# Kernel tuning notes

Measured on AMD Instinct MI355X. Metric: run time of the kernel, lower is better.

Reference implementation:

```python
import jax, jax.numpy as jnp
import numpy as np

H = 2048   # hidden_dim
E = 8      # num_experts
K = 2      # top_k
N = 4096   # tokens


def setup_inputs() -> dict:
    key = jax.random.key(0)
    ks = jax.random.split(key, 8)
    scale = 0.02
    return {
        "x": jax.random.normal(ks[0], (N, H), dtype=jnp.float32),
        # gate: torch Linear(H, E) -> weight [E, H], bias [E]
        "gate_W": jax.random.normal(ks[1], (E, H), dtype=jnp.float32) * scale,
        "gate_b": jnp.zeros((E,), dtype=jnp.float32),
        # per-expert 2-layer MLP; stored as [E, in, out] for direct einsum
        "W1": jax.random.normal(ks[2], (E, H, H), dtype=jnp.float32) * scale,
        "b1": jnp.zeros((E, H), dtype=jnp.float32),
        "W2": jax.random.normal(ks[3], (E, H, H), dtype=jnp.float32) * scale,
        "b2": jnp.zeros((E, H), dtype=jnp.float32),
    }


def reference(x, gate_W, gate_b, W1, b1, W2, b2):
    # gate softmax over experts: [N, E]
    gate_scores = jax.nn.softmax(x @ gate_W.T + gate_b, axis=-1)
    topk_scores, topk_idx = jax.lax.top_k(gate_scores, K)  # [N, K]
    n = x.shape[0]
    # combine weights: score at selected experts, 0 elsewhere -> [N, E]
    combine = jnp.zeros_like(gate_scores).at[
        jnp.arange(n)[:, None], topk_idx
    ].set(topk_scores)
    # dense per-expert MLP: h [N, E, H]
    h = jax.nn.relu(jnp.einsum('nh,ehf->nef', x, W1) + b1)
    out_e = jnp.einsum('nef,efg->neg', h, W2) + b2  # [N, E, H]
    aggregated = jnp.einsum('ne,neh->nh', combine, out_e)  # [N, H]
    return aggregated, gate_scores
```

## Files before the change

kernel.cpp:

```cpp
#include <hip/hip_runtime.h>
#include <hip/hip_bf16.h>

#define N_TOK 4096
#define HD    2048
#define NE    8

#define BM 128
#define BN 256
#define BK 32
#define NKS (HD/BK)
#define MAXROWS (N_TOK*2 + NE*BM)
#define TMAX (MAXROWS/BM)
#define NNT  (HD/BN)
#define NWG  (TMAX*NNT)
#define TSZ  ((BM+BN)*BK*2)

#define NCOPY 64

typedef __attribute__((ext_vector_type(4))) float f32x4;
typedef __attribute__((ext_vector_type(8))) short short8;
typedef __attribute__((ext_vector_type(8))) unsigned short ushort8;

typedef unsigned short u16;
typedef unsigned int   u32;


__device__ __forceinline__ float bf2f(u16 u) {
  union { u32 i; float f; } c; c.i = ((u32)u) << 16; return c.f;
}
__device__ __forceinline__ u16 f2bf(float f) {
  u32 x = __float_as_uint(f);
  u32 r = (x + 0x7fffu + ((x >> 16) & 1u)) >> 16;
  return (u16)r;
}

__device__ __forceinline__ void gload_lds16(const void* gsrc, void* ldst) {
  __builtin_amdgcn_global_load_lds(
      (const __attribute__((address_space(1))) u32*)gsrc,
      (__attribute__((address_space(3))) u32*)ldst, 16, 0, 0);
}

__global__ __launch_bounds__(256) void convert_transpose_kernel(
    const float* __restrict__ W1, const float* __restrict__ W2,
    u16* __restrict__ W1T, u16* __restrict__ W2T) {
  __shared__ float tile[64][65];
  int z = blockIdx.z;
  const float* W = (z < NE) ? W1 : W2;
  u16* WT = (z < NE) ? W1T : W2T;
  int e = z & 7;
  size_t ebase = (size_t)e * HD * HD;
  int n0 = blockIdx.x * 64;
  int k0 = blockIdx.y * 64;
  int t = threadIdx.x;
  int l = t & 63, w = t >> 6;
  #pragma unroll
  for (int jr = 0; jr < 4; ++jr) {
    int r = w*16 + jr*4 + (l >> 4);
    int cc = (l & 15) * 4;
    f32x4 v = *reinterpret_cast<const f32x4*>(W + ebase + (size_t)(k0 + r) * HD + n0 + cc);
    tile[r][cc+0] = v[0]; tile[r][cc+1] = v[1];
    tile[r][cc+2] = v[2]; tile[r][cc+3] = v[3];
  }
  __syncthreads();
  #pragma unroll
  for (int ps = 0; ps < 2; ++ps) {
    int np = ps*32 + (t >> 3);
    int kc = (t & 7) * 8;
    ushort8 v;
    #pragma unroll
    for (int j = 0; j < 8; ++j) v[j] = f2bf(tile[kc + j][np]);
    *reinterpret_cast<ushort8*>(WT + ebase + (size_t)(n0 + np) * HD + k0 + kc) = v;
  }
}

__global__ __launch_bounds__(256) void gate_kernel(
    const float* __restrict__ x, const float* __restrict__ gW, const float* __restrict__ gb,
    float* __restrict__ gate_out, int* __restrict__ cnt,
    int* __restrict__ picks, float* __restrict__ wts) {
  int wid = (blockIdx.x << 2) + (threadIdx.x >> 6);
  int lane = threadIdx.x & 63;
  int copy = blockIdx.x & (NCOPY-1);
  const float* xr = x + (size_t)wid * HD;
  float s[NE] = {};
  for (int k = 0; k < HD; k += 256) {
    f32x4 xv = *reinterpret_cast<const f32x4*>(xr + k + lane*4);
    #pragma unroll
    for (int e = 0; e < NE; ++e) {
      f32x4 wv = *reinterpret_cast<const f32x4*>(gW + (size_t)e*HD + k + lane*4);
      s[e] += xv[0]*wv[0] + xv[1]*wv[1] + xv[2]*wv[2] + xv[3]*wv[3];
    }
  }
  #pragma unroll
  for (int e = 0; e < NE; ++e) {
    float v = s[e];
    #pragma unroll
    for (int off = 32; off > 0; off >>= 1) v += __shfl_xor(v, off);
    s[e] = v + gb[e];
  }
  float mx = s[0];
  #pragma unroll
  for (int e = 1; e < NE; ++e) mx = fmaxf(mx, s[e]);
  float sum = 0.f;
  #pragma unroll
  for (int e = 0; e < NE; ++e) { s[e] = expf(s[e] - mx); sum += s[e]; }
  float inv = 1.f / sum;
  #pragma unroll
  for (int e = 0; e < NE; ++e) s[e] *= inv;
  int e0 = 0; float v0 = s[0];
  #pragma unroll
  for (int e = 1; e < NE; ++e) if (s[e] > v0) { v0 = s[e]; e0 = e; }
  int e1 = -1; float v1 = -1.f;
  #pragma unroll
  for (int e = 0; e < NE; ++e) if (e != e0 && s[e] > v1) { v1 = s[e]; e1 = e; }
  if (lane == 0) {
    #pragma unroll
    for (int e = 0; e < NE; ++e) gate_out[(size_t)wid*NE + e] = s[e];
    int p0 = atomicAdd(&cnt[copy*8 + e0], 1);
    int p1 = atomicAdd(&cnt[copy*8 + e1], 1);
    picks[wid*2]   = (p0 << 9) | (copy << 3) | e0;
    picks[wid*2+1] = (p1 << 9) | (copy << 3) | e1;
    wts[wid*2]   = v0;
    wts[wid*2+1] = v1;
  }
}

__global__ void scan_kernel(int* meta) {
  int e = threadIdx.x;
  if (e < NE) {
    int run = 0;
    for (int c = 0; c < NCOPY; ++c) {
      meta[512 + c*8 + e] = run;
      run += meta[c*8 + e];
    }
    meta[1024 + e] = run;
  }
}

__global__ void fill_kernel(const int* __restrict__ picks, const int* __restrict__ meta,
                            int* __restrict__ slot, int* __restrict__ rowTok) {
  int i = blockIdx.x * 256 + threadIdx.x;
  if (i >= N_TOK*2) return;
  int p = picks[i];
  int e = p & 7, c = (p >> 3) & (NCOPY-1), pos = p >> 9;
  int base = 0;
  #pragma unroll
  for (int ee = 0; ee < NE; ++ee)
    if (ee < e) base += ((meta[1024+ee] + BM - 1) >> 7) << 7;
  int row = base + meta[512 + c*8 + e] + pos;
  slot[i] = row;
  rowTok[row] = i >> 1;
}

__global__ __launch_bounds__(256) void gather_kernel(
    const float* __restrict__ x, const int* __restrict__ rowTok,
    u16* __restrict__ Xg) {
  int row = blockIdx.x;
  int tok = rowTok[row];
  int c = threadIdx.x * 8;
  ushort8 v;
  if (tok >= 0) {
    const f32x4* src = reinterpret_cast<const f32x4*>(x + (size_t)tok * HD + c);
    f32x4 a = src[0], b = src[1];
    #pragma unroll
    for (int j = 0; j < 4; ++j) { v[j] = f2bf(a[j]); v[4+j] = f2bf(b[j]); }
  } else {
    #pragma unroll
    for (int j = 0; j < 8; ++j) v[j] = 0;
  }
  *reinterpret_cast<ushort8*>(Xg + (size_t)row * HD + c) = v;
}

__device__ __forceinline__ void stage_tile(char* ldsbuf, const u16* Ak, const u16* Bk, int tid) {
  {
    int r = tid >> 2;
    int c = (tid & 3) ^ ((r >> 1) & 3);
    gload_lds16(Ak + (size_t)r*HD + c*8, ldsbuf + tid*16);
  }
  #pragma unroll
  for (int i = 0; i < 2; ++i) {
    int L = i*512 + tid;
    int r = L >> 2;
    int c = (L & 3) ^ ((r >> 1) & 3);
    gload_lds16(Bk + (size_t)r*HD + c*8, ldsbuf + BM*BK*2 + L*16);
  }
}

__device__ __forceinline__ void compute_ktile(
    const char* ldsA, const char* ldsB, f32x4 (&acc)[4][4],
    int wr, int wc, int l15, int lhi) {
  short8 af[4], bfr[4];
  #pragma unroll
  for (int m = 0; m < 4; ++m) {
    int r = wr*64 + m*16 + l15;
    int c = lhi ^ ((r >> 1) & 3);
    af[m] = *reinterpret_cast<const short8*>(ldsA + r*64 + c*16);
  }
  #pragma unroll
  for (int n = 0; n < 4; ++n) {
    int r = wc*64 + n*16 + l15;
    int c = lhi ^ ((r >> 1) & 3);
    bfr[n] = *reinterpret_cast<const short8*>(ldsB + r*64 + c*16);
  }
  #pragma unroll
  for (int m = 0; m < 4; ++m)
    #pragma unroll
    for (int n = 0; n < 4; ++n)
      acc[m][n] = __builtin_amdgcn_mfma_f32_16x16x32_bf16(af[m], bfr[n], acc[m][n], 0, 0, 0);
}

template<bool RELU>
__global__ __launch_bounds__(512, 4) void moe_gemm_kernel(
    const u16* __restrict__ A,
    const u16* __restrict__ WT,
    const float* __restrict__ bias,
    u16* __restrict__ Out,
    const int* __restrict__ tot) {
  int bid = blockIdx.x;
  int wg = (bid & 7) * (NWG/8) + (bid >> 3);
  int t  = wg >> 3;
  int nt = wg & 7;
  int tiles = 0, rows = 0, e = 0, tstart = 0, rbase = 0;
  #pragma unroll
  for (int i = 0; i < NE; ++i) {
    int tl = (tot[i] + BM - 1) >> 7;
    if (t >= tiles && t < tiles + tl) { e = i; tstart = tiles; rbase = rows; }
    tiles += tl; rows += tl << 7;
  }
  if (t >= tiles) return;
  int rowBase = rbase + (t - tstart) * BM;

  const u16* Ap = A + (size_t)rowBase * HD;
  const u16* Bp = WT + ((size_t)e * HD + (size_t)nt * BN) * HD;

  __shared__ char lds[3*TSZ];

  int tid = threadIdx.x;
  int lane = tid & 63;
  int wv = tid >> 6;
  int wr = wv >> 2, wc = wv & 3;
  int l15 = lane & 15, lhi = lane >> 4;

  f32x4 acc[4][4] = {};

  stage_tile(lds,       Ap,      Bp,      tid);
  stage_tile(lds + TSZ, Ap + BK, Bp + BK, tid);

  int rd = 0;
  for (int ks = 0; ks < NKS - 2; ++ks) {
    asm volatile("s_waitcnt vmcnt(3)" ::: "memory");
    __builtin_amdgcn_s_barrier();
    int wi = rd + 2; if (wi >= 3) wi -= 3;
    stage_tile(lds + wi*TSZ, Ap + (ks+2)*BK, Bp + (ks+2)*BK, tid);
    __builtin_amdgcn_sched_barrier(0);
    compute_ktile(lds + rd*TSZ, lds + rd*TSZ + BM*BK*2, acc, wr, wc, l15, lhi);
    if (++rd == 3) rd = 0;
  }
  asm volatile("s_waitcnt vmcnt(3)" ::: "memory");
  __builtin_amdgcn_s_barrier();
  compute_ktile(lds + rd*TSZ, lds + rd*TSZ + BM*BK*2, acc, wr, wc, l15, lhi);
  if (++rd == 3) rd = 0;
  asm volatile("s_waitcnt vmcnt(0)" ::: "memory");
  __builtin_amdgcn_s_barrier();
  compute_ktile(lds + rd*TSZ, lds + rd*TSZ + BM*BK*2, acc, wr, wc, l15, lhi);

  int orow = rowBase + wr*64;
  int ocol = nt*BN + wc*64;
  const float* bp = bias + (size_t)e * HD + ocol;
  #pragma unroll
  for (int n = 0; n < 4; ++n) {
    float bv = bp[n*16 + l15];
    #pragma unroll
    for (int m = 0; m < 4; ++m) {
      #pragma unroll
      for (int j = 0; j < 4; ++j) {
        float v = acc[m][n][j] + bv;
        if (RELU) v = fmaxf(v, 0.f);
        Out[(size_t)(orow + m*16 + lhi*4 + j) * HD + (ocol + n*16 + l15)] = f2bf(v);
      }
    }
  }
}

__global__ __launch_bounds__(256) void combine_kernel(
    const u16* __restrict__ Y, const int* __restrict__ slot,
    const float* __restrict__ wts, float* __restrict__ out) {
  int n = blockIdx.x;
  int r0 = slot[n*2], r1 = slot[n*2+1];
  float w0 = wts[n*2], w1 = wts[n*2+1];
  int c = threadIdx.x * 8;
  ushort8 y0 = *reinterpret_cast<const ushort8*>(Y + (size_t)r0*HD + c);
  ushort8 y1 = *reinterpret_cast<const ushort8*>(Y + (size_t)r1*HD + c);
  f32x4 o0, o1;
  #pragma unroll
  for (int j = 0; j < 4; ++j) {
    o0[j] = w0*bf2f(y0[j])   + w1*bf2f(y1[j]);
    o1[j] = w0*bf2f(y0[4+j]) + w1*bf2f(y1[4+j]);
  }
  f32x4* dst = reinterpret_cast<f32x4*>(out + (size_t)n*HD + c);
  dst[0] = o0; dst[1] = o1;
}

extern "C" void kernel_launch(void* const* d_in, const int* in_sizes, int n_in,
                              void* d_out, int out_size, void* d_ws, size_t ws_size,
                              hipStream_t stream) {
  const float* x     = (const float*)d_in[0];
  const float* gateW = (const float*)d_in[1];
  const float* gateb = (const float*)d_in[2];
  const float* W1    = (const float*)d_in[3];
  const float* b1    = (const float*)d_in[4];
  const float* W2    = (const float*)d_in[5];
  const float* b2    = (const float*)d_in[6];
  float* out      = (float*)d_out;
  float* gate_out = out + (size_t)N_TOK * HD;

  char* ws = (char*)d_ws;
  size_t o = 0;
  u16* W1T = (u16*)(ws + o); o += (size_t)NE*HD*HD*2;
  u16* W2T = (u16*)(ws + o); o += (size_t)NE*HD*HD*2;
  u16* Xg  = (u16*)(ws + o);
  u16* Y   = Xg;
  o += (size_t)MAXROWS*HD*2;
  u16* Hbuf = (u16*)(ws + o); o += (size_t)MAXROWS*HD*2;
  int*   meta   = (int*)(ws + o);   o += 8192;
  int*   picks  = (int*)(ws + o);   o += (size_t)N_TOK*2*4;
  float* wts    = (float*)(ws + o); o += (size_t)N_TOK*2*4;
  int*   slot   = (int*)(ws + o);   o += (size_t)N_TOK*2*4;
  int*   rowTok = (int*)(ws + o);   o += (size_t)MAXROWS*4;

  hipMemsetAsync(meta, 0, NCOPY*8*4, stream);
  hipMemsetAsync(rowTok, 0xFF, (size_t)MAXROWS*4, stream);

  convert_transpose_kernel<<<dim3(HD/64, HD/64, 2*NE), 256, 0, stream>>>(W1, W2, W1T, W2T);
  gate_kernel<<<N_TOK/4, 256, 0, stream>>>(x, gateW, gateb, gate_out, meta, picks, wts);
  scan_kernel<<<1, 64, 0, stream>>>(meta);
  fill_kernel<<<(N_TOK*2)/256, 256, 0, stream>>>(picks, meta, slot, rowTok);
  gather_kernel<<<MAXROWS, 256, 0, stream>>>(x, rowTok, Xg);
  moe_gemm_kernel<true ><<<dim3(NWG), 512, 0, stream>>>(Xg,   W1T, b1, Hbuf, meta + 1024);
  moe_gemm_kernel<false><<<dim3(NWG), 512, 0, stream>>>(Hbuf, W2T, b2, Y,    meta + 1024);
  combine_kernel<<<N_TOK, 256, 0, stream>>>(Y, slot, wts, out);
}
```

Baseline: 323.2 us.

## Deepen GEMM LDS pipeline to five buffers with split-phase interleaved loads and MFMAs

Moves the expert GEMM main loop from a 3-buffer, 2-ahead prefetch to a 5-buffer ring that prefetches 3 k-tiles ahead. Each k-step is split into two phases: LDS fragment reads and global-to-LDS loads are interleaved with half of the MFMAs, separated by extra barriers, and the MFMA sections run under raised s_setprio. The aim is to hide global load latency better and keep the matrix units busy. In exchange, occupancy is lowered (launch bounds 4 to 2 and more LDS per block), and the extra barriers per k-step add synchronisation cost.

```diff
diff --git a/kernel.cpp b/kernel.cpp
--- a/kernel.cpp
+++ b/kernel.cpp
@@ -14,6 +14,7 @@
 #define NNT  (HD/BN)
 #define NWG  (TMAX*NNT)
 #define TSZ  ((BM+BN)*BK*2)
+#define NBUF 5
 
 #define NCOPY 64
 
@@ -170,46 +171,20 @@
   *reinterpret_cast<ushort8*>(Xg + (size_t)row * HD + c) = v;
 }
 
-__device__ __forceinline__ void stage_tile(char* ldsbuf, const u16* Ak, const u16* Bk, int tid) {
-  {
-    int r = tid >> 2;
-    int c = (tid & 3) ^ ((r >> 1) & 3);
-    gload_lds16(Ak + (size_t)r*HD + c*8, ldsbuf + tid*16);
-  }
-  #pragma unroll
-  for (int i = 0; i < 2; ++i) {
-    int L = i*512 + tid;
-    int r = L >> 2;
-    int c = (L & 3) ^ ((r >> 1) & 3);
-    gload_lds16(Bk + (size_t)r*HD + c*8, ldsbuf + BM*BK*2 + L*16);
-  }
-}
-
-__device__ __forceinline__ void compute_ktile(
-    const char* ldsA, const char* ldsB, f32x4 (&acc)[4][4],
-    int wr, int wc, int l15, int lhi) {
-  short8 af[4], bfr[4];
-  #pragma unroll
-  for (int m = 0; m < 4; ++m) {
-    int r = wr*64 + m*16 + l15;
-    int c = lhi ^ ((r >> 1) & 3);
-    af[m] = *reinterpret_cast<const short8*>(ldsA + r*64 + c*16);
-  }
-  #pragma unroll
-  for (int n = 0; n < 4; ++n) {
-    int r = wc*64 + n*16 + l15;
-    int c = lhi ^ ((r >> 1) & 3);
-    bfr[n] = *reinterpret_cast<const short8*>(ldsB + r*64 + c*16);
-  }
-  #pragma unroll
-  for (int m = 0; m < 4; ++m)
-    #pragma unroll
-    for (int n = 0; n < 4; ++n)
-      acc[m][n] = __builtin_amdgcn_mfma_f32_16x16x32_bf16(af[m], bfr[n], acc[m][n], 0, 0, 0);
+__device__ __forceinline__ void stage_A(char* ldsbuf, const u16* Ak, int tid) {
+  int r = tid >> 2;
+  int c = (tid & 3) ^ ((r >> 1) & 3);
+  gload_lds16(Ak + (size_t)r*HD + c*8, ldsbuf + tid*16);
+}
+__device__ __forceinline__ void stage_B(char* ldsbuf, const u16* Bk, int tid, int i) {
+  int L = i*512 + tid;
+  int r = L >> 2;
+  int c = (L & 3) ^ ((r >> 1) & 3);
+  gload_lds16(Bk + (size_t)r*HD + c*8, ldsbuf + BM*BK*2 + L*16);
 }
 
 template<bool RELU>
-__global__ __launch_bounds__(512, 4) void moe_gemm_kernel(
+__global__ __launch_bounds__(512, 2) void moe_gemm_kernel(
     const u16* __restrict__ A,
     const u16* __restrict__ WT,
     const float* __restrict__ bias,
@@ -232,7 +207,7 @@
   const u16* Ap = A + (size_t)rowBase * HD;
   const u16* Bp = WT + ((size_t)e * HD + (size_t)nt * BN) * HD;
 
-  __shared__ char lds[3*TSZ];
+  __shared__ char lds[NBUF*TSZ];
 
   int tid = threadIdx.x;
   int lane = tid & 63;
@@ -242,26 +217,78 @@
 
   f32x4 acc[4][4] = {};
 
-  stage_tile(lds,       Ap,      Bp,      tid);
-  stage_tile(lds + TSZ, Ap + BK, Bp + BK, tid);
-
-  int rd = 0;
-  for (int ks = 0; ks < NKS - 2; ++ks) {
-    asm volatile("s_waitcnt vmcnt(3)" ::: "memory");
+  #pragma unroll
+  for (int p = 0; p < 3; ++p) {
+    stage_A(lds + p*TSZ, Ap + p*BK, tid);
+    stage_B(lds + p*TSZ, Bp + p*BK, tid, 0);
+    stage_B(lds + p*TSZ, Bp + p*BK, tid, 1);
+  }
+
+  int rd = 0, wi = 3;
+  for (int ks = 0; ks < NKS; ++ks) {
+    if (ks < NKS-2)       asm volatile("s_waitcnt vmcnt(6)" ::: "memory");
+    else if (ks == NKS-2) asm volatile("s_waitcnt vmcnt(3)" ::: "memory");
+    else                  asm volatile("s_waitcnt vmcnt(0)" ::: "memory");
     __builtin_amdgcn_s_barrier();
-    int wi = rd + 2; if (wi >= 3) wi -= 3;
-    stage_tile(lds + wi*TSZ, Ap + (ks+2)*BK, Bp + (ks+2)*BK, tid);
-    __builtin_amdgcn_sched_barrier(0);
-    compute_ktile(lds + rd*TSZ, lds + rd*TSZ + BM*BK*2, acc, wr, wc, l15, lhi);
-    if (++rd == 3) rd = 0;
-  }
-  asm volatile("s_waitcnt vmcnt(3)" ::: "memory");
-  __builtin_amdgcn_s_barrier();
-  compute_ktile(lds + rd*TSZ, lds + rd*TSZ + BM*BK*2, acc, wr, wc, l15, lhi);
-  if (++rd == 3) rd = 0;
-  asm volatile("s_waitcnt vmcnt(0)" ::: "memory");
-  __builtin_amdgcn_s_barrier();
-  compute_ktile(lds + rd*TSZ, lds + rd*TSZ + BM*BK*2, acc, wr, wc, l15, lhi);
+    __builtin_amdgcn_sched_barrier(0);
+
+    const char* bufA = lds + rd*TSZ;
+    const char* bufB = bufA + BM*BK*2;
+    char* wbuf = lds + wi*TSZ;
+    bool issue = (ks + 3 < NKS);
+    const u16* Aq = Ap + (ks+3)*BK;
+    const u16* Bq = Bp + (ks+3)*BK;
+
+    short8 af[4], bfr[4];
+    #pragma unroll
+    for (int m = 0; m < 4; ++m) {
+      int r = wr*64 + m*16 + l15;
+      int c = lhi ^ ((r >> 1) & 3);
+      af[m] = *reinterpret_cast<const short8*>(bufA + r*64 + c*16);
+    }
+    #pragma unroll
+    for (int n = 0; n < 2; ++n) {
+      int r = wc*64 + n*16 + l15;
+      int c = lhi ^ ((r >> 1) & 3);
+      bfr[n] = *reinterpret_cast<const short8*>(bufB + r*64 + c*16);
+    }
+    if (issue) { stage_A(wbuf, Aq, tid); stage_B(wbuf, Bq, tid, 0); }
+    __builtin_amdgcn_sched_barrier(0);
+    __builtin_amdgcn_s_barrier();
+    __builtin_amdgcn_sched_barrier(0);
+    __builtin_amdgcn_s_setprio(1);
+    #pragma unroll
+    for (int m = 0; m < 4; ++m)
+      #pragma unroll
+      for (int n = 0; n < 2; ++n)
+        acc[m][n] = __builtin_amdgcn_mfma_f32_16x16x32_bf16(af[m], bfr[n], acc[m][n], 0, 0, 0);
+    __builtin_amdgcn_s_setprio(0);
+    __builtin_amdgcn_sched_barrier(0);
+    __builtin_amdgcn_s_barrier();
+    __builtin_amdgcn_sched_barrier(0);
+
+    #pragma unroll
+    for (int n = 2; n < 4; ++n) {
+      int r = wc*64 + n*16 + l15;
+      int c = lhi ^ ((r >> 1) & 3);
+      bfr[n] = *reinterpret_cast<const short8*>(bufB + r*64 + c*16);
+    }
+    if (issue) stage_B(wbuf, Bq, tid, 1);
+    __builtin_amdgcn_sched_barrier(0);
+    __builtin_amdgcn_s_barrier();
+    __builtin_amdgcn_sched_barrier(0);
+    __builtin_amdgcn_s_setprio(1);
+    #pragma unroll
+    for (int m = 0; m < 4; ++m)
+      #pragma unroll
+      for (int n = 2; n < 4; ++n)
+        acc[m][n] = __builtin_amdgcn_mfma_f32_16x16x32_bf16(af[m], bfr[n], acc[m][n], 0, 0, 0);
+    __builtin_amdgcn_s_setprio(0);
+    __builtin_amdgcn_sched_barrier(0);
+
+    if (++rd == NBUF) rd = 0;
+    if (++wi == NBUF) wi = 0;
+  }
 
   int orow = rowBase + wr*64;
   int ocol = nt*BN + wc*64;
```

After: 371.6 us. +15.0%, slower.
